# Optimization experiments

Measured on AMD Instinct MI355X. Metric: run time of the kernel, lower is better.

The kernel has to match this reference:

```python
import jax, jax.numpy as jnp
import numpy as np

B, V, C, H, W, D = 1, 3, 32, 320, 320, 32


def setup_inputs() -> dict:
    key = jax.random.key(0)
    ks = jax.random.split(key, 14)
    feats = jax.random.normal(ks[0], (B, V, C, H, W), jnp.float32)
    # Valid pinhole projections: P = [[K @ [R|t]], [0,0,0,1]], identity rotation,
    # horizontal baselines sized so the warp stays mostly in-image over the depth range.
    K = np.array([[400.0, 0.0, W / 2.0], [0.0, 400.0, H / 2.0], [0.0, 0.0, 1.0]])
    mats = []
    for tx in (0.0, 100.0, -100.0):
        Rt = np.eye(4)
        Rt[0, 3] = tx
        P = np.eye(4)
        P[:3, :4] = K @ Rt[:3, :4]
        mats.append(P)
    proj = jnp.asarray(np.broadcast_to(np.stack(mats)[None], (B, V, 4, 4)).copy(), jnp.float32)
    planes = jnp.linspace(425.0, 935.0, D, dtype=jnp.float32)
    depth_values = jnp.broadcast_to(planes[None, :, None, None], (B, D, H, W)).astype(jnp.float32)
    s = 0.05  # small init so exp(reg_cost) stays well-scaled
    W0 = s * jax.random.normal(ks[1], (8, C, 3, 3), jnp.float32)
    Ws1 = s * jax.random.normal(ks[2], (8, 8, 3, 3), jnp.float32)
    W1 = s * jax.random.normal(ks[3], (16, 8, 3, 3), jnp.float32)
    Ws2 = s * jax.random.normal(ks[4], (16, 16, 3, 3), jnp.float32)
    W2 = s * jax.random.normal(ks[5], (32, 16, 3, 3), jnp.float32)
    Ws3 = s * jax.random.normal(ks[6], (32, 32, 3, 3), jnp.float32)
    W3 = s * jax.random.normal(ks[7], (64, 32, 3, 3), jnp.float32)
    Ws4 = s * jax.random.normal(ks[8], (64, 64, 3, 3), jnp.float32)
    U4 = s * jax.random.normal(ks[9], (32, 64, 1, 1), jnp.float32)
    U3 = s * jax.random.normal(ks[10], (16, 32, 1, 1), jnp.float32)
    U2 = s * jax.random.normal(ks[11], (8, 16, 1, 1), jnp.float32)
    Wout = s * jax.random.normal(ks[12], (1, 8, 3, 3), jnp.float32)
    return dict(feats=feats, proj=proj, depth_values=depth_values, W0=W0, Ws1=Ws1,
                W1=W1, Ws2=Ws2, W2=W2, Ws3=Ws3, W3=W3, Ws4=Ws4, U4=U4, U3=U3, U2=U2, Wout=Wout)


def _conv(x, w, stride=1):
    return jax.lax.conv_general_dilated(x, w, (stride, stride), 'SAME',
                                        dimension_numbers=('NCHW', 'OIHW', 'NCHW'))


def _up2(x):
    return jnp.repeat(jnp.repeat(x, 2, axis=2), 2, axis=3)


def _bilinear(img, x, y):
    # img [C,H,W]; x,y [N] pixel coords; zero padding, align_corners semantics
    Cc, Hh, Ww = img.shape
    x0 = jnp.floor(x)
    y0 = jnp.floor(y)
    wx = x - x0
    wy = y - y0

    def tap(xi, yi):
        valid = ((xi >= 0) & (xi <= Ww - 1) & (yi >= 0) & (yi <= Hh - 1)).astype(img.dtype)
        xc = jnp.clip(xi, 0, Ww - 1).astype(jnp.int32)
        yc = jnp.clip(yi, 0, Hh - 1).astype(jnp.int32)
        return img[:, yc, xc] * valid  # [C,N]

    return (tap(x0, y0) * (1 - wx) * (1 - wy) + tap(x0 + 1, y0) * wx * (1 - wy)
            + tap(x0, y0 + 1) * (1 - wx) * wy + tap(x0 + 1, y0 + 1) * wx * wy)


def _forward(feats, proj, depth_values, W0, Ws1, W1, Ws2, W2, Ws3, W3, Ws4, U4, U3, U2, Wout):
    Bn, Vn, Cn, Hn, Wn = feats.shape
    Dn = depth_values.shape[1]
    N = Hn * Wn
    relu = jax.nn.relu
    ref = feats[:, 0]
    ref_sq = ref * ref
    # Precompute per-src-view rotated pixel rays and translations.
    inv_ref = jnp.linalg.inv(proj[:, 0])                       # [B,4,4]
    rel = jnp.einsum('bvij,bjk->bvik', proj[:, 1:], inv_ref)   # [B,V-1,4,4]
    rot, trans = rel[:, :, :3, :3], rel[:, :, :3, 3]
    ys, xs = jnp.meshgrid(jnp.arange(Hn), jnp.arange(Wn), indexing='ij')
    pix = jnp.stack([xs.ravel(), ys.ravel(), jnp.ones(N)], 0).astype(feats.dtype)  # [3,N]
    rot_pix = jnp.einsum('bvij,jn->bvin', rot, pix)            # [B,V-1,3,N]

    def regularize(x, s1, s2, s3, s4):
        c1 = relu(_conv(x, W0) + _conv(s1, Ws1))
        c2 = relu(_conv(c1, W1, 2) + _conv(s2, Ws2))
        c3 = relu(_conv(c2, W2, 2) + _conv(s3, Ws3))
        c4 = relu(_conv(c3, W3, 2) + _conv(s4, Ws4))
        u3 = c3 + _up2(_conv(c4, U4))
        u2 = c2 + _up2(_conv(u3, U3))
        u1 = c1 + _up2(_conv(u2, U2))
        return _conv(u1, Wout), c1, c2, c3, c4

    def step(carry, depth_slice):  # depth_slice [B,H,W]
        s1, s2, s3, s4, exp_sum, depth_img, max_prob = carry
        vol_sum, vol_sq = ref, ref_sq
        dflat = depth_slice.reshape(Bn, 1, N)
        for v in range(Vn - 1):
            xyz = rot_pix[:, v] * dflat + trans[:, v, :, None]   # [B,3,N]
            px = xyz[:, 0] / xyz[:, 2]
            py = xyz[:, 1] / xyz[:, 2]
            warped = jax.vmap(_bilinear)(feats[:, v + 1], px, py).reshape(Bn, Cn, Hn, Wn)
            vol_sum = vol_sum + warped
            vol_sq = vol_sq + warped * warped
        variance = vol_sq / Vn - (vol_sum / Vn) ** 2
        cost, s1, s2, s3, s4 = regularize(variance, s1, s2, s3, s4)
        prob = jnp.exp(cost)                                     # [B,1,H,W]
        max_prob = jnp.maximum(max_prob, prob)                   # == flag*prob + (1-flag)*max
        depth_img = depth_img + depth_slice[:, None] * prob
        exp_sum = exp_sum + prob
        return (s1, s2, s3, s4, exp_sum, depth_img, max_prob), None

    z = lambda c, h, w: jnp.zeros((Bn, c, h, w), feats.dtype)
    init = (z(8, Hn, Wn), z(16, Hn // 2, Wn // 2), z(32, Hn // 4, Wn // 4), z(64, Hn // 8, Wn // 8),
            z(1, Hn, Wn), z(1, Hn, Wn), z(1, Hn, Wn))
    carry, _ = jax.lax.scan(step, init, jnp.moveaxis(depth_values, 1, 0))
    _, _, _, _, exp_sum, depth_img, max_prob = carry
    es = exp_sum + 1e-10
    depth_map = (depth_img / es)[:, 0]
    prob_map = (max_prob / es)[:, 0]
    return jnp.stack([depth_map, prob_map], axis=1)  # [B,2,H,W]


def reference(feats, proj, depth_values, W0, Ws1, W1, Ws2, W2, Ws3, W3, Ws4, U4, U3, U2, Wout):
    return _forward(feats, proj, depth_values, W0, Ws1, W1, Ws2, W2, Ws3, W3, Ws4, U4, U3, U2, Wout)
```

## Files before the change

### kernel.cpp

```cpp
#include <hip/hip_runtime.h>
#include <hip/hip_fp16.h>
#include <math.h>

#define HH 320
#define WW 320
#define NP (HH*WW)
#define CC 32
#define DD 32

#define H2 160
#define W2 160
#define N2 (H2*W2)
#define H4 80
#define W4 80
#define N4 (H4*W4)
#define H8 40
#define W8 40
#define N8 (H8*W8)

#define HALO 18
#define NHALO (HALO*HALO)

#define C1SZ (8*NP)
#define C2SZ (16*N2)
#define C3SZ (32*N4)
#define C4SZ (64*N8)

#define SMEM_FLOATS 5344

#define OFF_REL   0
#define OFF_C1R   64
#define OFF_C2R   (OFF_C1R + 5*C1SZ)
#define OFF_C3R   (OFF_C2R + 4*C2SZ)
#define OFF_C4R   (OFF_C3R + 3*C3SZ)
#define OFF_ESUM  (OFF_C4R + 2*C4SZ)
#define OFF_DIMG  (OFF_ESUM + NP)
#define OFF_MAXP  (OFF_DIMG + NP)
#define OFF_ACCE  (OFF_MAXP + NP)
#define OFF_FT    OFF_ACCE
#define OFF_END   (OFF_FT + (3*CC*NP)/2)

__global__ void k_prep(const float* __restrict__ proj, float* __restrict__ rel) {
    if (threadIdx.x != 0 || blockIdx.x != 0) return;
    float a[4][4], inv[4][4];
#pragma unroll
    for (int i = 0; i < 4; i++)
#pragma unroll
        for (int j = 0; j < 4; j++) {
            a[i][j] = proj[i*4 + j];
            inv[i][j] = (i == j) ? 1.0f : 0.0f;
        }
#pragma unroll
    for (int c = 0; c < 4; c++) {
        float s = 1.0f / a[c][c];
#pragma unroll
        for (int j = 0; j < 4; j++) { a[c][j] *= s; inv[c][j] *= s; }
#pragma unroll
        for (int r = 0; r < 4; r++) if (r != c) {
            float f = a[r][c];
#pragma unroll
            for (int j = 0; j < 4; j++) {
                a[r][j] -= f * a[c][j];
                inv[r][j] -= f * inv[c][j];
            }
        }
    }
#pragma unroll
    for (int v = 1; v < 3; v++) {
        const float* P = proj + v*16;
        float rm[3][4];
#pragma unroll
        for (int i = 0; i < 3; i++)
#pragma unroll
            for (int j = 0; j < 4; j++) {
                float s = 0.0f;
#pragma unroll
                for (int k = 0; k < 4; k++) s += P[i*4 + k] * inv[k][j];
                rm[i][j] = s;
            }
        float* o = rel + (v-1)*12;
        o[0]=rm[0][0]; o[1]=rm[0][1]; o[2]=rm[0][2];
        o[3]=rm[1][0]; o[4]=rm[1][1]; o[5]=rm[1][2];
        o[6]=rm[2][0]; o[7]=rm[2][1]; o[8]=rm[2][2];
        o[9]=rm[0][3]; o[10]=rm[1][3]; o[11]=rm[2][3];
    }
}

__global__ __launch_bounds__(256) void k_transpose(const float* __restrict__ feats,
                                                   __half* __restrict__ featsT) {
    __shared__ float lds[32][65];
    int g = blockIdx.x;
    int v = g / 1600;
    int p0 = (g - v*1600) * 64;
    const float* src = feats + (size_t)v*CC*NP + p0;
    for (int i = threadIdx.x; i < 32*64; i += 256) {
        int c = i >> 6, pp = i & 63;
        lds[c][pp] = src[(size_t)c*NP + pp];
    }
    __syncthreads();
    __half* dst = featsT + ((size_t)v*NP + p0)*32;
    int pp = threadIdx.x >> 2, cq = (threadIdx.x & 3) * 8;
    __half2 h[4];
#pragma unroll
    for (int j = 0; j < 4; j++)
        h[j] = __floats2half2_rn(lds[cq+2*j][pp], lds[cq+2*j+1][pp]);
    *(float4*)(dst + (size_t)pp*32 + cq) = *(float4*)h;
}

__device__ __forceinline__ void set_line_h(const __half* base, float* s) {
    const float4* q = (const float4*)base;
#pragma unroll
    for (int i = 0; i < 4; i++) {
        float4 raw = q[i];
        const __half2* h2 = (const __half2*)&raw;
#pragma unroll
        for (int j = 0; j < 4; j++) {
            float2 f = __half22float2(h2[j]);
            s[i*8 + 2*j]     = f.x;
            s[i*8 + 2*j + 1] = f.y;
        }
    }
}
__device__ __forceinline__ void acc_line_h(const __half* base, float w, float* t) {
    const float4* q = (const float4*)base;
#pragma unroll
    for (int i = 0; i < 4; i++) {
        float4 raw = q[i];
        const __half2* h2 = (const __half2*)&raw;
#pragma unroll
        for (int j = 0; j < 4; j++) {
            float2 f = __half22float2(h2[j]);
            t[i*8 + 2*j]     += f.x * w;
            t[i*8 + 2*j + 1] += f.y * w;
        }
    }
}

__device__ __forceinline__ int band_tile(int blk) {
    return (blk & 7) * 50 + (blk >> 3);
}


__device__ void stageA(int blk, int d, int useT,
        const float* __restrict__ feats, const __half* __restrict__ featsT,
        const float* __restrict__ rel,
        const float* __restrict__ depthv, const float* __restrict__ c1r,
        const float* __restrict__ W0, const float* __restrict__ Ws1,
        float* smem) {
    __half2* pbuf = (__half2*)smem;
    float* fbuf = smem;
    const float* dslice = depthv + (size_t)d * NP;
    const float* s1 = c1r + (size_t)((d+4)%5) * C1SZ;
    float* c1out = (float*)c1r + (size_t)(d%5) * C1SZ;

    int L = band_tile(blk);
    int bx = L % 20, by = L / 20;
    int ox0 = bx*16, oy0 = by*16;

    const float* f1 = feats + CC*NP;
    const float* f2 = feats + 2*CC*NP;
    const __half* fT0 = featsT;
    const __half* fT1 = featsT + (size_t)CC*NP;
    const __half* fT2 = featsT + (size_t)2*CC*NP;
    const float inv3 = 1.0f / 3.0f;

    int opx = threadIdx.x & 15, opy = threadIdx.x >> 4;
    int obase = opy*HALO + opx;
    int outp = (oy0 + opy)*WW + ox0 + opx;

    for (int s = 0; s < 2; s++) {
        int hp = threadIdx.x + s*256;
        if (hp >= NHALO) break;
        int hy = hp / HALO, hx = hp - hy*HALO;
        int gy = oy0 + hy - 1, gx = ox0 + hx - 1;
        if (gy < 0 || gy >= HH || gx < 0 || gx >= WW) {
            __half2 z = __floats2half2_rn(0.0f, 0.0f);
#pragma unroll 8
            for (int c = 0; c < 16; c++) pbuf[c*NHALO + hp] = z;
            continue;
        }
        int p = gy*WW + gx;
        float depth = dslice[p];
        float fx = (float)gx, fy = (float)gy;
        int offs[8]; float wts[8];
#pragma unroll
        for (int v = 0; v < 2; v++) {
            const float* r = rel + v*12;
            float X = (r[0]*fx + r[1]*fy + r[2]) * depth + r[9];
            float Y = (r[3]*fx + r[4]*fy + r[5]) * depth + r[10];
            float Z = (r[6]*fx + r[7]*fy + r[8]) * depth + r[11];
            float iz = 1.0f / Z;
            float px = X * iz, py = Y * iz;
            float x0f = floorf(px), y0f = floorf(py);
            float wx = px - x0f, wy = py - y0f;
            int x0 = (int)x0f, y0 = (int)y0f;
#pragma unroll
            for (int t = 0; t < 4; t++) {
                int xi = x0 + (t & 1), yi = y0 + (t >> 1);
                float wgt = ((t & 1) ? wx : 1.0f - wx) * ((t >> 1) ? wy : 1.0f - wy);
                bool valid = (xi >= 0) && (xi <= WW-1) && (yi >= 0) && (yi <= HH-1);
                int xc = min(max(xi, 0), WW-1);
                int yc = min(max(yi, 0), HH-1);
                offs[v*4 + t] = yc*WW + xc;
                wts[v*4 + t] = valid ? wgt : 0.0f;
            }
        }

        float var[32];
        if (useT) {
            float sum[32], sq[32], t[32];
            set_line_h(fT0 + ((size_t)p << 5), sum);
#pragma unroll
            for (int c = 0; c < 32; c++) sq[c] = sum[c]*sum[c];
#pragma unroll
            for (int c = 0; c < 32; c++) t[c] = 0.0f;
#pragma unroll
            for (int tp = 0; tp < 4; tp++)
                acc_line_h(fT1 + ((size_t)offs[tp] << 5), wts[tp], t);
#pragma unroll
            for (int c = 0; c < 32; c++) { sum[c] += t[c]; sq[c] += t[c]*t[c]; }
#pragma unroll
            for (int c = 0; c < 32; c++) t[c] = 0.0f;
#pragma unroll
            for (int tp = 0; tp < 4; tp++)
                acc_line_h(fT2 + ((size_t)offs[4+tp] << 5), wts[4+tp], t);
#pragma unroll
            for (int c = 0; c < 32; c++) { sum[c] += t[c]; sq[c] += t[c]*t[c]; }
#pragma unroll
            for (int c = 0; c < 32; c++) {
                float m = sum[c] * inv3;
                var[c] = sq[c] * inv3 - m*m;
            }
        } else {
            for (int c = 0; c < 32; c++) {
                float rv = feats[c*NP + p];
                const float* b1 = f1 + c*NP;
                float t1 = b1[offs[0]]*wts[0] + b1[offs[1]]*wts[1]
                         + b1[offs[2]]*wts[2] + b1[offs[3]]*wts[3];
                const float* b2 = f2 + c*NP;
                float t2 = b2[offs[4]]*wts[4] + b2[offs[5]]*wts[5]
                         + b2[offs[6]]*wts[6] + b2[offs[7]]*wts[7];
                float sum = rv + t1 + t2;
                float sq  = rv*rv + t1*t1 + t2*t2;
                float m = sum * inv3;
                var[c] = sq * inv3 - m*m;
            }
        }
#pragma unroll
        for (int c = 0; c < 16; c++)
            pbuf[c*NHALO + hp] = __floats2half2_rn(var[2*c], var[2*c+1]);
    }
    __syncthreads();

    float acc[8];
#pragma unroll
    for (int o = 0; o < 8; o++) acc[o] = 0.0f;

    for (int cp = 0; cp < 16; cp++) {
        float t0[9], t1[9];
#pragma unroll
        for (int ky = 0; ky < 3; ky++)
#pragma unroll
            for (int kx = 0; kx < 3; kx++) {
                __half2 h = pbuf[cp*NHALO + obase + ky*HALO + kx];
                t0[ky*3+kx] = __low2float(h);
                t1[ky*3+kx] = __high2float(h);
            }
#pragma unroll
        for (int o = 0; o < 8; o++) {
            const float* w0 = W0 + (o*32 + 2*cp)*9;
            float a = acc[o];
#pragma unroll
            for (int k = 0; k < 9; k++) a += t0[k] * w0[k];
#pragma unroll
            for (int k = 0; k < 9; k++) a += t1[k] * w0[9 + k];
            acc[o] = a;
        }
    }
    __syncthreads();

    for (int hp = threadIdx.x; hp < NHALO; hp += 256) {
        int hy = hp / HALO, hx = hp - hy*HALO;
        int gy = oy0 + hy - 1, gx = ox0 + hx - 1;
        bool v = (gy >= 0) && (gy < HH) && (gx >= 0) && (gx < WW);
        int p = v ? gy*WW + gx : 0;
#pragma unroll
        for (int c = 0; c < 8; c++) fbuf[c*NHALO + hp] = v ? s1[c*NP + p] : 0.0f;
    }
    __syncthreads();
    for (int ci = 0; ci < 8; ci++) {
        float t[9];
#pragma unroll
        for (int ky = 0; ky < 3; ky++)
#pragma unroll
            for (int kx = 0; kx < 3; kx++) t[ky*3+kx] = fbuf[ci*NHALO + obase + ky*HALO + kx];
#pragma unroll
        for (int o = 0; o < 8; o++) {
            const float* w = Ws1 + (o*8 + ci)*9;
            float a = acc[o];
#pragma unroll
            for (int k = 0; k < 9; k++) a += t[k] * w[k];
            acc[o] = a;
        }
    }
#pragma unroll
    for (int o = 0; o < 8; o++) c1out[o*NP + outp] = fmaxf(acc[o], 0.0f);
}

__device__ void stageB(int blk, int d,
        const float* __restrict__ c1r, const float* __restrict__ c2r_,
        const float* __restrict__ W1, const float* __restrict__ Ws2) {
    const float* c1 = c1r + (size_t)(d%5) * C1SZ;
    const float* s2 = c2r_ + (size_t)((d+3)%4) * C2SZ;
    float* c2 = (float*)c2r_ + (size_t)(d%4) * C2SZ;
    int p = (blk % 100)*256 + threadIdx.x;
    if (p >= N2) return;
    int og = blk / 100;
    int y = p / W2, x = p - y*W2;
    int offsA[9]; float mskA[9];
#pragma unroll
    for (int k = 0; k < 9; k++) {
        int yy = 2*y + k/3, xx = 2*x + k%3;
        bool v = (yy < HH) && (xx < WW);
        offsA[k] = v ? yy*WW + xx : 0;
        mskA[k] = v ? 1.0f : 0.0f;
    }
    int offsB[9]; float mskB[9];
#pragma unroll
    for (int k = 0; k < 9; k++) {
        int yy = y + k/3 - 1, xx = x + k%3 - 1;
        bool v = (yy >= 0) && (yy < H2) && (xx >= 0) && (xx < W2);
        offsB[k] = v ? yy*W2 + xx : 0;
        mskB[k] = v ? 1.0f : 0.0f;
    }
    float acc[8];
#pragma unroll
    for (int o = 0; o < 8; o++) acc[o] = 0.0f;
    for (int ci = 0; ci < 8; ci++) {
        const float* b = c1 + ci*NP;
        float t[9];
#pragma unroll
        for (int k = 0; k < 9; k++) t[k] = b[offsA[k]] * mskA[k];
#pragma unroll
        for (int o = 0; o < 8; o++) {
            const float* w = W1 + ((og*8 + o)*8 + ci)*9;
            float a = acc[o];
#pragma unroll
            for (int k = 0; k < 9; k++) a += t[k] * w[k];
            acc[o] = a;
        }
    }
    for (int ci = 0; ci < 16; ci++) {
        const float* b = s2 + ci*N2;
        float t[9];
#pragma unroll
        for (int k = 0; k < 9; k++) t[k] = b[offsB[k]] * mskB[k];
#pragma unroll
        for (int o = 0; o < 8; o++) {
            const float* w = Ws2 + ((og*8 + o)*16 + ci)*9;
            float a = acc[o];
#pragma unroll
            for (int k = 0; k < 9; k++) a += t[k] * w[k];
            acc[o] = a;
        }
    }
#pragma unroll
    for (int o = 0; o < 8; o++) c2[(og*8 + o)*N2 + p] = fmaxf(acc[o], 0.0f);
}

__device__ void stageC(int blk, int d,
        const float* __restrict__ c2r_, const float* __restrict__ c3r_,
        const float* __restrict__ W2w, const float* __restrict__ Ws3) {
    const float* c2 = c2r_ + (size_t)(d%4) * C2SZ;
    const float* s3 = c3r_ + (size_t)((d+2)%3) * C3SZ;
    float* c3 = (float*)c3r_ + (size_t)(d%3) * C3SZ;
    int p = (blk % 25)*256 + threadIdx.x;
    if (p >= N4) return;
    int og = blk / 25;
    int y = p / W4, x = p - y*W4;
    int offsA[9]; float mskA[9];
#pragma unroll
    for (int k = 0; k < 9; k++) {
        int yy = 2*y + k/3, xx = 2*x + k%3;
        bool v = (yy < H2) && (xx < W2);
        offsA[k] = v ? yy*W2 + xx : 0;
        mskA[k] = v ? 1.0f : 0.0f;
    }
    int offsB[9]; float mskB[9];
#pragma unroll
    for (int k = 0; k < 9; k++) {
        int yy = y + k/3 - 1, xx = x + k%3 - 1;
        bool v = (yy >= 0) && (yy < H4) && (xx >= 0) && (xx < W4);
        offsB[k] = v ? yy*W4 + xx : 0;
        mskB[k] = v ? 1.0f : 0.0f;
    }
    float acc[8];
#pragma unroll
    for (int o = 0; o < 8; o++) acc[o] = 0.0f;
    for (int ci = 0; ci < 16; ci++) {
        const float* b = c2 + ci*N2;
        float t[9];
#pragma unroll
        for (int k = 0; k < 9; k++) t[k] = b[offsA[k]] * mskA[k];
#pragma unroll
        for (int o = 0; o < 8; o++) {
            const float* w = W2w + ((og*8 + o)*16 + ci)*9;
            float a = acc[o];
#pragma unroll
            for (int k = 0; k < 9; k++) a += t[k] * w[k];
            acc[o] = a;
        }
    }
    for (int ci = 0; ci < 32; ci++) {
        const float* b = s3 + ci*N4;
        float t[9];
#pragma unroll
        for (int k = 0; k < 9; k++) t[k] = b[offsB[k]] * mskB[k];
#pragma unroll
        for (int o = 0; o < 8; o++) {
            const float* w = Ws3 + ((og*8 + o)*32 + ci)*9;
            float a = acc[o];
#pragma unroll
            for (int k = 0; k < 9; k++) a += t[k] * w[k];
            acc[o] = a;
        }
    }
#pragma unroll
    for (int o = 0; o < 8; o++) c3[(og*8 + o)*N4 + p] = fmaxf(acc[o], 0.0f);
}

__device__ void stageD(int blk, int d,
        const float* __restrict__ c3r_, const float* __restrict__ c4r_,
        const float* __restrict__ W3w, const float* __restrict__ Ws4) {
    const float* c3 = c3r_ + (size_t)(d%3) * C3SZ;
    const float* s4 = c4r_ + (size_t)((d+1)%2) * C4SZ;
    float* c4 = (float*)c4r_ + (size_t)(d%2) * C4SZ;
    int p = (blk % 7)*256 + threadIdx.x;
    if (p >= N8) return;
    int og = blk / 7;
    int y = p / W8, x = p - y*W8;
    int offsA[9]; float mskA[9];
#pragma unroll
    for (int k = 0; k < 9; k++) {
        int yy = 2*y + k/3, xx = 2*x + k%3;
        bool v = (yy < H4) && (xx < W4);
        offsA[k] = v ? yy*W4 + xx : 0;
        mskA[k] = v ? 1.0f : 0.0f;
    }
    int offsB[9]; float mskB[9];
#pragma unroll
    for (int k = 0; k < 9; k++) {
        int yy = y + k/3 - 1, xx = x + k%3 - 1;
        bool v = (yy >= 0) && (yy < H8) && (xx >= 0) && (xx < W8);
        offsB[k] = v ? yy*W8 + xx : 0;
        mskB[k] = v ? 1.0f : 0.0f;
    }
    float acc[8];
#pragma unroll
    for (int o = 0; o < 8; o++) acc[o] = 0.0f;
    for (int ci = 0; ci < 32; ci++) {
        const float* b = c3 + ci*N4;
        float t[9];
#pragma unroll
        for (int k = 0; k < 9; k++) t[k] = b[offsA[k]] * mskA[k];
#pragma unroll
        for (int o = 0; o < 8; o++) {
            const float* w = W3w + ((og*8 + o)*32 + ci)*9;
            float a = acc[o];
#pragma unroll
            for (int k = 0; k < 9; k++) a += t[k] * w[k];
            acc[o] = a;
        }
    }
    for (int ci = 0; ci < 64; ci++) {
        const float* b = s4 + ci*N8;
        float t[9];
#pragma unroll
        for (int k = 0; k < 9; k++) t[k] = b[offsB[k]] * mskB[k];
#pragma unroll
        for (int o = 0; o < 8; o++) {
            const float* w = Ws4 + ((og*8 + o)*64 + ci)*9;
            float a = acc[o];
#pragma unroll
            for (int k = 0; k < 9; k++) a += t[k] * w[k];
            acc[o] = a;
        }
    }
#pragma unroll
    for (int o = 0; o < 8; o++) c4[(og*8 + o)*N8 + p] = fmaxf(acc[o], 0.0f);
}

__device__ void stageU(int blk, int d,
        const float* __restrict__ c1r, const float* __restrict__ c2r_,
        const float* __restrict__ c3r_, const float* __restrict__ c4r_,
        const float* __restrict__ U4, const float* __restrict__ U3,
        const float* __restrict__ U2, const float* __restrict__ Wout,
        const float* __restrict__ depthv,
        float* __restrict__ exp_sum, float* __restrict__ depth_img,
        float* __restrict__ max_prob, float* smem) {
    const float* c1 = c1r + (size_t)(d%5) * C1SZ;
    const float* c2 = c2r_ + (size_t)(d%4) * C2SZ;
    const float* c3 = c3r_ + (size_t)(d%3) * C3SZ;
    const float* c4 = c4r_ + (size_t)(d%2) * C4SZ;
    const float* dslice = depthv + (size_t)d * NP;
    float* u3s = smem;
    float* u2s = smem + 32*36;
    float* u1s = smem + 32*36 + 16*100;

    int L = band_tile(blk);
    int bx = L % 20, by = L / 20;
    int ox0 = bx*16, oy0 = by*16;
    int qy0 = (oy0 >> 2) - 1, qx0 = (ox0 >> 2) - 1;
    int hy0 = (oy0 >> 1) - 1, hx0 = (ox0 >> 1) - 1;

    for (int i = threadIdx.x; i < 32*36; i += 256) {
        int ch = i / 36, pp = i - ch*36;
        int y4 = qy0 + pp/6, x4 = qx0 + pp%6;
        int y4c = min(max(y4, 0), H4-1), x4c = min(max(x4, 0), W4-1);
        int pl = (y4c >> 1)*W8 + (x4c >> 1);
        const float* w = U4 + ch*64;
        float s = c3[ch*N4 + y4c*W4 + x4c];
#pragma unroll 8
        for (int ci = 0; ci < 64; ci++) s += c4[ci*N8 + pl] * w[ci];
        u3s[ch*36 + pp] = s;
    }
    __syncthreads();
    for (int i = threadIdx.x; i < 16*100; i += 256) {
        int ch = i / 100, pp = i - ch*100;
        int y2 = hy0 + pp/10, x2 = hx0 + pp%10;
        int y2c = min(max(y2, 0), H2-1), x2c = min(max(x2, 0), W2-1);
        int ly = (y2c >> 1) - qy0, lx = (x2c >> 1) - qx0;
        const float* w = U3 + ch*32;
        float s = c2[ch*N2 + y2c*W2 + x2c];
#pragma unroll 8
        for (int ci = 0; ci < 32; ci++) s += u3s[ci*36 + ly*6 + lx] * w[ci];
        u2s[ch*100 + pp] = s;
    }
    __syncthreads();
    for (int i = threadIdx.x; i < 8*NHALO; i += 256) {
        int ch = i / NHALO, pp = i - ch*NHALO;
        int gy = oy0 + pp/HALO - 1, gx = ox0 + pp%HALO - 1;
        float s = 0.0f;
        if (gy >= 0 && gy < HH && gx >= 0 && gx < WW) {
            int ly = (gy >> 1) - hy0, lx = (gx >> 1) - hx0;
            const float* w = U2 + ch*16;
            s = c1[ch*NP + gy*WW + gx];
#pragma unroll
            for (int ci = 0; ci < 16; ci++) s += u2s[ci*100 + ly*10 + lx] * w[ci];
        }
        u1s[ch*NHALO + pp] = s;
    }
    __syncthreads();
    int px = threadIdx.x & 15, py = threadIdx.x >> 4;
    int base = py*HALO + px;
    float cost = 0.0f;
#pragma unroll
    for (int ci = 0; ci < 8; ci++) {
        const float* w = Wout + ci*9;
#pragma unroll
        for (int ky = 0; ky < 3; ky++)
#pragma unroll
            for (int kx = 0; kx < 3; kx++)
                cost += u1s[ci*NHALO + base + ky*HALO + kx] * w[ky*3 + kx];
    }
    int p = (oy0 + py)*WW + ox0 + px;
    float prob = expf(cost);
    exp_sum[p] += prob;
    depth_img[p] += dslice[p] * prob;
    max_prob[p] = fmaxf(max_prob[p], prob);
}

__global__ __launch_bounds__(256) void k_uber(
        int t, int useT,
        const float* __restrict__ feats, const __half* __restrict__ featsT,
        const float* __restrict__ rel,
        const float* __restrict__ depthv,
        const float* __restrict__ W0, const float* __restrict__ Ws1,
        const float* __restrict__ W1, const float* __restrict__ Ws2,
        const float* __restrict__ W2w, const float* __restrict__ Ws3,
        const float* __restrict__ W3w, const float* __restrict__ Ws4,
        const float* __restrict__ U4, const float* __restrict__ U3,
        const float* __restrict__ U2, const float* __restrict__ Wout,
        float* __restrict__ c1r, float* __restrict__ c2r,
        float* __restrict__ c3r, float* __restrict__ c4r,
        float* __restrict__ esum, float* __restrict__ dimg,
        float* __restrict__ maxp) {
    __shared__ float smem[SMEM_FLOATS];
    int b = blockIdx.x;
    if (b < 400) {
        int d = t;
        if (d < DD) stageA(b, d, useT, feats, featsT, rel, depthv, c1r, W0, Ws1, smem);
    } else if (b < 600) {
        int d = t - 1;
        if (d >= 0 && d < DD) stageB(b - 400, d, c1r, c2r, W1, Ws2);
    } else if (b < 700) {
        int d = t - 2;
        if (d >= 0 && d < DD) stageC(b - 600, d, c2r, c3r, W2w, Ws3);
    } else if (b < 756) {
        int d = t - 3;
        if (d >= 0 && d < DD) stageD(b - 700, d, c3r, c4r, W3w, Ws4);
    } else {
        int d = t - 4;
        if (d >= 0 && d < DD)
            stageU(b - 756, d, c1r, c2r, c3r, c4r, U4, U3, U2, Wout, depthv,
                   esum, dimg, maxp, smem);
    }
}

__global__ __launch_bounds__(256) void k_final(
        const float* __restrict__ exp_sum, const float* __restrict__ depth_img,
        const float* __restrict__ max_prob, float* __restrict__ out) {
    int p = blockIdx.x*256 + threadIdx.x;
    if (p >= NP) return;
    float es = exp_sum[p] + 1e-10f;
    out[p] = depth_img[p] / es;
    out[NP + p] = max_prob[p] / es;
}

extern "C" void kernel_launch(void* const* d_in, const int* in_sizes, int n_in,
                              void* d_out, int out_size, void* d_ws, size_t ws_size,
                              hipStream_t stream) {
    const float* feats = (const float*)d_in[0];
    const float* proj  = (const float*)d_in[1];
    const float* depthv= (const float*)d_in[2];
    const float* W0  = (const float*)d_in[3];
    const float* Ws1 = (const float*)d_in[4];
    const float* W1  = (const float*)d_in[5];
    const float* Ws2 = (const float*)d_in[6];
    const float* W2w = (const float*)d_in[7];
    const float* Ws3 = (const float*)d_in[8];
    const float* W3w = (const float*)d_in[9];
    const float* Ws4 = (const float*)d_in[10];
    const float* U4  = (const float*)d_in[11];
    const float* U3  = (const float*)d_in[12];
    const float* U2  = (const float*)d_in[13];
    const float* Wout= (const float*)d_in[14];

    float* ws = (float*)d_ws;
    float* rel  = ws + OFF_REL;
    float* c1r  = ws + OFF_C1R;
    float* c2r  = ws + OFF_C2R;
    float* c3r  = ws + OFF_C3R;
    float* c4r  = ws + OFF_C4R;
    float* esum = ws + OFF_ESUM;
    float* dimg = ws + OFF_DIMG;
    float* maxp = ws + OFF_MAXP;

    int useT = (ws_size >= (size_t)OFF_END * sizeof(float)) ? 1 : 0;
    __half* featsT = (__half*)(useT ? (ws + OFF_FT) : ws);

    hipMemsetAsync(c1r, 0, (size_t)(OFF_ACCE - OFF_C1R) * sizeof(float), stream);
    k_prep<<<1, 1, 0, stream>>>(proj, rel);
    if (useT)
        k_transpose<<<dim3(3*1600), 256, 0, stream>>>(feats, featsT);

    for (int t = 0; t < DD + 4; t++) {
        k_uber<<<dim3(1156), 256, 0, stream>>>(t, useT, feats, featsT, rel, depthv,
            W0, Ws1, W1, Ws2, W2w, Ws3, W3w, Ws4, U4, U3, U2, Wout,
            c1r, c2r, c3r, c4r, esum, dimg, maxp);
    }
    k_final<<<dim3(400), 256, 0, stream>>>(esum, dimg, maxp, (float*)d_out);
}
```

Baseline: 3.176 ms.

## Split variance warp out of conv stage into separate pipelined stage

Stage A's homography warp and variance computation now run as their own pipeline stage. Each thread handles one pixel and 16 channels, writing an fp16 variance volume into a double-buffered workspace. The conv stage then just loads halo tiles from that buffer, which removes the redundant warp work the old code did on halo pixels and raises parallelism in the first stage. In exchange the pipeline gains one more step and one more launch, the grid grows, and each depth slice needs an extra global write and read of roughly 6.5 MB.

```diff
diff --git a/kernel.cpp b/kernel.cpp
--- a/kernel.cpp
+++ b/kernel.cpp
@@ -37,7 +37,9 @@
 #define OFF_DIMG  (OFF_ESUM + NP)
 #define OFF_MAXP  (OFF_DIMG + NP)
 #define OFF_ACCE  (OFF_MAXP + NP)
-#define OFF_FT    OFF_ACCE
+#define VARSZ_F   ((CC*NP)/2)
+#define OFF_VARR  OFF_ACCE
+#define OFF_FT    (OFF_VARR + 2*VARSZ_F)
 #define OFF_END   (OFF_FT + (3*CC*NP)/2)
 
 __global__ void k_prep(const float* __restrict__ proj, float* __restrict__ rel) {
@@ -107,10 +109,10 @@
     *(float4*)(dst + (size_t)pp*32 + cq) = *(float4*)h;
 }
 
-__device__ __forceinline__ void set_line_h(const __half* base, float* s) {
+__device__ __forceinline__ void set_hline16(const __half* base, float* s) {
     const float4* q = (const float4*)base;
 #pragma unroll
-    for (int i = 0; i < 4; i++) {
+    for (int i = 0; i < 2; i++) {
         float4 raw = q[i];
         const __half2* h2 = (const __half2*)&raw;
 #pragma unroll
@@ -121,10 +123,10 @@
         }
     }
 }
-__device__ __forceinline__ void acc_line_h(const __half* base, float w, float* t) {
+__device__ __forceinline__ void acc_hline16(const __half* base, float w, float* t) {
     const float4* q = (const float4*)base;
 #pragma unroll
-    for (int i = 0; i < 4; i++) {
+    for (int i = 0; i < 2; i++) {
         float4 raw = q[i];
         const __half2* h2 = (const __half2*)&raw;
 #pragma unroll
@@ -136,119 +138,127 @@
     }
 }
 
-__device__ __forceinline__ int band_tile(int blk) {
-    return (blk & 7) * 50 + (blk >> 3);
-}
-
-
-__device__ void stageA(int blk, int d, int useT,
+__device__ __forceinline__ int band_tile(int blk)  { return (blk & 7) * 50  + (blk >> 3); }
+__device__ __forceinline__ int band_chunk(int blk) { return (blk & 7) * 100 + (blk >> 3); }
+
+
+__device__ void stageAvar(int blk, int d, int useT,
         const float* __restrict__ feats, const __half* __restrict__ featsT,
-        const float* __restrict__ rel,
-        const float* __restrict__ depthv, const float* __restrict__ c1r,
+        const float* __restrict__ rel, const float* __restrict__ depthv,
+        __half* __restrict__ varR) {
+    int chunk = band_chunk(blk);
+    int p = chunk * 128 + (threadIdx.x & 127);
+    int half = threadIdx.x >> 7;
+    int cb = half * 16;
+    const float* dslice = depthv + (size_t)d * NP;
+    float depth = dslice[p];
+    int gy = p / WW, gx = p - gy*WW;
+    float fx = (float)gx, fy = (float)gy;
+    int offs[8]; float wts[8];
+#pragma unroll
+    for (int v = 0; v < 2; v++) {
+        const float* r = rel + v*12;
+        float X = (r[0]*fx + r[1]*fy + r[2]) * depth + r[9];
+        float Y = (r[3]*fx + r[4]*fy + r[5]) * depth + r[10];
+        float Z = (r[6]*fx + r[7]*fy + r[8]) * depth + r[11];
+        float iz = 1.0f / Z;
+        float px = X * iz, py = Y * iz;
+        float x0f = floorf(px), y0f = floorf(py);
+        float wx = px - x0f, wy = py - y0f;
+        int x0 = (int)x0f, y0 = (int)y0f;
+#pragma unroll
+        for (int t = 0; t < 4; t++) {
+            int xi = x0 + (t & 1), yi = y0 + (t >> 1);
+            float wgt = ((t & 1) ? wx : 1.0f - wx) * ((t >> 1) ? wy : 1.0f - wy);
+            bool valid = (xi >= 0) && (xi <= WW-1) && (yi >= 0) && (yi <= HH-1);
+            int xc = min(max(xi, 0), WW-1);
+            int yc = min(max(yi, 0), HH-1);
+            offs[v*4 + t] = yc*WW + xc;
+            wts[v*4 + t] = valid ? wgt : 0.0f;
+        }
+    }
+
+    const float inv3 = 1.0f / 3.0f;
+    float sum[16], sq[16], t[16], var[16];
+    if (useT) {
+        const __half* fT0 = featsT;
+        const __half* fT1 = featsT + (size_t)CC*NP;
+        const __half* fT2 = featsT + (size_t)2*CC*NP;
+        set_hline16(fT0 + ((size_t)p << 5) + cb, sum);
+#pragma unroll
+        for (int c = 0; c < 16; c++) sq[c] = sum[c]*sum[c];
+#pragma unroll
+        for (int c = 0; c < 16; c++) t[c] = 0.0f;
+#pragma unroll
+        for (int tp = 0; tp < 4; tp++)
+            acc_hline16(fT1 + ((size_t)offs[tp] << 5) + cb, wts[tp], t);
+#pragma unroll
+        for (int c = 0; c < 16; c++) { sum[c] += t[c]; sq[c] += t[c]*t[c]; }
+#pragma unroll
+        for (int c = 0; c < 16; c++) t[c] = 0.0f;
+#pragma unroll
+        for (int tp = 0; tp < 4; tp++)
+            acc_hline16(fT2 + ((size_t)offs[4+tp] << 5) + cb, wts[4+tp], t);
+#pragma unroll
+        for (int c = 0; c < 16; c++) { sum[c] += t[c]; sq[c] += t[c]*t[c]; }
+    } else {
+        const float* f1 = feats + CC*NP;
+        const float* f2 = feats + 2*CC*NP;
+        for (int c = 0; c < 16; c++) {
+            float rv = feats[(cb+c)*NP + p];
+            const float* b1 = f1 + (cb+c)*NP;
+            float t1 = b1[offs[0]]*wts[0] + b1[offs[1]]*wts[1]
+                     + b1[offs[2]]*wts[2] + b1[offs[3]]*wts[3];
+            const float* b2 = f2 + (cb+c)*NP;
+            float t2 = b2[offs[4]]*wts[4] + b2[offs[5]]*wts[5]
+                     + b2[offs[6]]*wts[6] + b2[offs[7]]*wts[7];
+            sum[c] = rv + t1 + t2;
+            sq[c]  = rv*rv + t1*t1 + t2*t2;
+        }
+    }
+#pragma unroll
+    for (int c = 0; c < 16; c++) {
+        float m = sum[c] * inv3;
+        var[c] = sq[c] * inv3 - m*m;
+    }
+    __half2 o[8];
+#pragma unroll
+    for (int c = 0; c < 8; c++) o[c] = __floats2half2_rn(var[2*c], var[2*c+1]);
+    float4* dst = (float4*)(varR + (size_t)(d & 1) * (size_t)CC * NP
+                                  + ((size_t)p << 5) + cb);
+    dst[0] = ((float4*)o)[0];
+    dst[1] = ((float4*)o)[1];
+}
+
+__device__ void stageAconv(int blk, int d,
+        const __half* __restrict__ varR, const float* __restrict__ c1r,
         const float* __restrict__ W0, const float* __restrict__ Ws1,
         float* smem) {
     __half2* pbuf = (__half2*)smem;
     float* fbuf = smem;
-    const float* dslice = depthv + (size_t)d * NP;
     const float* s1 = c1r + (size_t)((d+4)%5) * C1SZ;
     float* c1out = (float*)c1r + (size_t)(d%5) * C1SZ;
+    const __half* vsrc = varR + (size_t)(d & 1) * (size_t)CC * NP;
 
     int L = band_tile(blk);
     int bx = L % 20, by = L / 20;
     int ox0 = bx*16, oy0 = by*16;
 
-    const float* f1 = feats + CC*NP;
-    const float* f2 = feats + 2*CC*NP;
-    const __half* fT0 = featsT;
-    const __half* fT1 = featsT + (size_t)CC*NP;
-    const __half* fT2 = featsT + (size_t)2*CC*NP;
-    const float inv3 = 1.0f / 3.0f;
-
     int opx = threadIdx.x & 15, opy = threadIdx.x >> 4;
     int obase = opy*HALO + opx;
     int outp = (oy0 + opy)*WW + ox0 + opx;
 
-    for (int s = 0; s < 2; s++) {
-        int hp = threadIdx.x + s*256;
-        if (hp >= NHALO) break;
+    for (int i = threadIdx.x; i < NHALO*4; i += 256) {
+        int hp = i >> 2, q = i & 3;
         int hy = hp / HALO, hx = hp - hy*HALO;
         int gy = oy0 + hy - 1, gx = ox0 + hx - 1;
-        if (gy < 0 || gy >= HH || gx < 0 || gx >= WW) {
-            __half2 z = __floats2half2_rn(0.0f, 0.0f);
-#pragma unroll 8
-            for (int c = 0; c < 16; c++) pbuf[c*NHALO + hp] = z;
-            continue;
-        }
-        int p = gy*WW + gx;
-        float depth = dslice[p];
-        float fx = (float)gx, fy = (float)gy;
-        int offs[8]; float wts[8];
-#pragma unroll
-        for (int v = 0; v < 2; v++) {
-            const float* r = rel + v*12;
-            float X = (r[0]*fx + r[1]*fy + r[2]) * depth + r[9];
-            float Y = (r[3]*fx + r[4]*fy + r[5]) * depth + r[10];
-            float Z = (r[6]*fx + r[7]*fy + r[8]) * depth + r[11];
-            float iz = 1.0f / Z;
-            float px = X * iz, py = Y * iz;
-            float x0f = floorf(px), y0f = floorf(py);
-            float wx = px - x0f, wy = py - y0f;
-            int x0 = (int)x0f, y0 = (int)y0f;
-#pragma unroll
-            for (int t = 0; t < 4; t++) {
-                int xi = x0 + (t & 1), yi = y0 + (t >> 1);
-                float wgt = ((t & 1) ? wx : 1.0f - wx) * ((t >> 1) ? wy : 1.0f - wy);
-                bool valid = (xi >= 0) && (xi <= WW-1) && (yi >= 0) && (yi <= HH-1);
-                int xc = min(max(xi, 0), WW-1);
-                int yc = min(max(yi, 0), HH-1);
-                offs[v*4 + t] = yc*WW + xc;
-                wts[v*4 + t] = valid ? wgt : 0.0f;
-            }
-        }
-
-        float var[32];
-        if (useT) {
-            float sum[32], sq[32], t[32];
-            set_line_h(fT0 + ((size_t)p << 5), sum);
-#pragma unroll
-            for (int c = 0; c < 32; c++) sq[c] = sum[c]*sum[c];
-#pragma unroll
-            for (int c = 0; c < 32; c++) t[c] = 0.0f;
-#pragma unroll
-            for (int tp = 0; tp < 4; tp++)
-                acc_line_h(fT1 + ((size_t)offs[tp] << 5), wts[tp], t);
-#pragma unroll
-            for (int c = 0; c < 32; c++) { sum[c] += t[c]; sq[c] += t[c]*t[c]; }
-#pragma unroll
-            for (int c = 0; c < 32; c++) t[c] = 0.0f;
-#pragma unroll
-            for (int tp = 0; tp < 4; tp++)
-                acc_line_h(fT2 + ((size_t)offs[4+tp] << 5), wts[4+tp], t);
-#pragma unroll
-            for (int c = 0; c < 32; c++) { sum[c] += t[c]; sq[c] += t[c]*t[c]; }
-#pragma unroll
-            for (int c = 0; c < 32; c++) {
-                float m = sum[c] * inv3;
-                var[c] = sq[c] * inv3 - m*m;
-            }
-        } else {
-            for (int c = 0; c < 32; c++) {
-                float rv = feats[c*NP + p];
-                const float* b1 = f1 + c*NP;
-                float t1 = b1[offs[0]]*wts[0] + b1[offs[1]]*wts[1]
-                         + b1[offs[2]]*wts[2] + b1[offs[3]]*wts[3];
-                const float* b2 = f2 + c*NP;
-                float t2 = b2[offs[4]]*wts[4] + b2[offs[5]]*wts[5]
-                         + b2[offs[6]]*wts[6] + b2[offs[7]]*wts[7];
-                float sum = rv + t1 + t2;
-                float sq  = rv*rv + t1*t1 + t2*t2;
-                float m = sum * inv3;
-                var[c] = sq * inv3 - m*m;
-            }
-        }
-#pragma unroll
-        for (int c = 0; c < 16; c++)
-            pbuf[c*NHALO + hp] = __floats2half2_rn(var[2*c], var[2*c+1]);
+        float4 v4 = make_float4(0.0f, 0.0f, 0.0f, 0.0f);
+        if (gy >= 0 && gy < HH && gx >= 0 && gx < WW)
+            v4 = *(const float4*)(vsrc + ((size_t)(gy*WW + gx) << 5) + q*8);
+        const __half2* h2 = (const __half2*)&v4;
+#pragma unroll
+        for (int j = 0; j < 4; j++)
+            pbuf[(q*4 + j)*NHALO + hp] = h2[j];
     }
     __syncthreads();
 
@@ -584,25 +594,28 @@
         float* __restrict__ c1r, float* __restrict__ c2r,
         float* __restrict__ c3r, float* __restrict__ c4r,
         float* __restrict__ esum, float* __restrict__ dimg,
-        float* __restrict__ maxp) {
+        float* __restrict__ maxp, __half* __restrict__ varR) {
     __shared__ float smem[SMEM_FLOATS];
     int b = blockIdx.x;
-    if (b < 400) {
+    if (b < 800) {
         int d = t;
-        if (d < DD) stageA(b, d, useT, feats, featsT, rel, depthv, c1r, W0, Ws1, smem);
-    } else if (b < 600) {
+        if (d < DD) stageAvar(b, d, useT, feats, featsT, rel, depthv, varR);
+    } else if (b < 1200) {
         int d = t - 1;
-        if (d >= 0 && d < DD) stageB(b - 400, d, c1r, c2r, W1, Ws2);
-    } else if (b < 700) {
+        if (d >= 0 && d < DD) stageAconv(b - 800, d, varR, c1r, W0, Ws1, smem);
+    } else if (b < 1400) {
         int d = t - 2;
-        if (d >= 0 && d < DD) stageC(b - 600, d, c2r, c3r, W2w, Ws3);
-    } else if (b < 756) {
+        if (d >= 0 && d < DD) stageB(b - 1200, d, c1r, c2r, W1, Ws2);
+    } else if (b < 1500) {
         int d = t - 3;
-        if (d >= 0 && d < DD) stageD(b - 700, d, c3r, c4r, W3w, Ws4);
+        if (d >= 0 && d < DD) stageC(b - 1400, d, c2r, c3r, W2w, Ws3);
+    } else if (b < 1556) {
+        int d = t - 4;
+        if (d >= 0 && d < DD) stageD(b - 1500, d, c3r, c4r, W3w, Ws4);
     } else {
-        int d = t - 4;
+        int d = t - 5;
         if (d >= 0 && d < DD)
-            stageU(b - 756, d, c1r, c2r, c3r, c4r, U4, U3, U2, Wout, depthv,
+            stageU(b - 1556, d, c1r, c2r, c3r, c4r, U4, U3, U2, Wout, depthv,
                    esum, dimg, maxp, smem);
     }
 }
@@ -645,6 +658,7 @@
     float* esum = ws + OFF_ESUM;
     float* dimg = ws + OFF_DIMG;
     float* maxp = ws + OFF_MAXP;
+    __half* varR = (__half*)(ws + OFF_VARR);
 
     int useT = (ws_size >= (size_t)OFF_END * sizeof(float)) ? 1 : 0;
     __half* featsT = (__half*)(useT ? (ws + OFF_FT) : ws);
@@ -654,10 +668,10 @@
     if (useT)
         k_transpose<<<dim3(3*1600), 256, 0, stream>>>(feats, featsT);
 
-    for (int t = 0; t < DD + 4; t++) {
-        k_uber<<<dim3(1156), 256, 0, stream>>>(t, useT, feats, featsT, rel, depthv,
+    for (int t = 0; t < DD + 5; t++) {
+        k_uber<<<dim3(1956), 256, 0, stream>>>(t, useT, feats, featsT, rel, depthv,
             W0, Ws1, W1, Ws2, W2w, Ws3, W3w, Ws4, U4, U3, U2, Wout,
-            c1r, c2r, c3r, c4r, esum, dimg, maxp);
+            c1r, c2r, c3r, c4r, esum, dimg, maxp, varR);
     }
     k_final<<<dim3(400), 256, 0, stream>>>(esum, dimg, maxp, (float*)d_out);
 }
```

Result: slower. 6.088 ms (+91.7%).

## Split stage A into 16x8 tiles with output-channel split across thread halves

Applied to the files above, without the earlier changes.

Stage A tiles shrink from 16x16 to 16x8, so twice as many blocks (800) run the warp/variance and first conv stage. The 180-pixel halo is now covered in a single pass by 256 threads, and the two halves of the block each compute 4 of the 8 output channels. This is meant to shorten the critical-path stage A block and spread its work across more CUs per pipeline step. The cost is more halo recomputation, since 180 halo pixels serve 128 outputs instead of 324 serving 256, and the launch grows to 1556 blocks.

```diff
diff --git a/kernel.cpp b/kernel.cpp
--- a/kernel.cpp
+++ b/kernel.cpp
@@ -17,6 +17,12 @@
 #define H8 40
 #define W8 40
 #define N8 (H8*W8)
+
+#define TAW 16
+#define TAH 8
+#define HAW 18
+#define HAH 10
+#define NHA (HAW*HAH)
 
 #define HALO 18
 #define NHALO (HALO*HALO)
@@ -136,9 +142,8 @@
     }
 }
 
-__device__ __forceinline__ int band_tile(int blk) {
-    return (blk & 7) * 50 + (blk >> 3);
-}
+__device__ __forceinline__ int band_tileU(int blk) { return (blk & 7) * 50  + (blk >> 3); }
+__device__ __forceinline__ int band_tileA(int blk) { return (blk & 7) * 100 + (blk >> 3); }
 
 
 __device__ void stageA(int blk, int d, int useT,
@@ -153,9 +158,9 @@
     const float* s1 = c1r + (size_t)((d+4)%5) * C1SZ;
     float* c1out = (float*)c1r + (size_t)(d%5) * C1SZ;
 
-    int L = band_tile(blk);
+    int L = band_tileA(blk);
     int bx = L % 20, by = L / 20;
-    int ox0 = bx*16, oy0 = by*16;
+    int ox0 = bx*TAW, oy0 = by*TAH;
 
     const float* f1 = feats + CC*NP;
     const float* f2 = feats + 2*CC*NP;
@@ -164,97 +169,96 @@
     const __half* fT2 = featsT + (size_t)2*CC*NP;
     const float inv3 = 1.0f / 3.0f;
 
-    int opx = threadIdx.x & 15, opy = threadIdx.x >> 4;
-    int obase = opy*HALO + opx;
-    int outp = (oy0 + opy)*WW + ox0 + opx;
-
-    for (int s = 0; s < 2; s++) {
-        int hp = threadIdx.x + s*256;
-        if (hp >= NHALO) break;
-        int hy = hp / HALO, hx = hp - hy*HALO;
+    int hp = threadIdx.x;
+    if (hp < NHA) {
+        int hy = hp / HAW, hx = hp - hy*HAW;
         int gy = oy0 + hy - 1, gx = ox0 + hx - 1;
         if (gy < 0 || gy >= HH || gx < 0 || gx >= WW) {
             __half2 z = __floats2half2_rn(0.0f, 0.0f);
 #pragma unroll 8
-            for (int c = 0; c < 16; c++) pbuf[c*NHALO + hp] = z;
-            continue;
-        }
-        int p = gy*WW + gx;
-        float depth = dslice[p];
-        float fx = (float)gx, fy = (float)gy;
-        int offs[8]; float wts[8];
-#pragma unroll
-        for (int v = 0; v < 2; v++) {
-            const float* r = rel + v*12;
-            float X = (r[0]*fx + r[1]*fy + r[2]) * depth + r[9];
-            float Y = (r[3]*fx + r[4]*fy + r[5]) * depth + r[10];
-            float Z = (r[6]*fx + r[7]*fy + r[8]) * depth + r[11];
-            float iz = 1.0f / Z;
-            float px = X * iz, py = Y * iz;
-            float x0f = floorf(px), y0f = floorf(py);
-            float wx = px - x0f, wy = py - y0f;
-            int x0 = (int)x0f, y0 = (int)y0f;
-#pragma unroll
-            for (int t = 0; t < 4; t++) {
-                int xi = x0 + (t & 1), yi = y0 + (t >> 1);
-                float wgt = ((t & 1) ? wx : 1.0f - wx) * ((t >> 1) ? wy : 1.0f - wy);
-                bool valid = (xi >= 0) && (xi <= WW-1) && (yi >= 0) && (yi <= HH-1);
-                int xc = min(max(xi, 0), WW-1);
-                int yc = min(max(yi, 0), HH-1);
-                offs[v*4 + t] = yc*WW + xc;
-                wts[v*4 + t] = valid ? wgt : 0.0f;
+            for (int c = 0; c < 16; c++) pbuf[c*NHA + hp] = z;
+        } else {
+            int p = gy*WW + gx;
+            float depth = dslice[p];
+            float fx = (float)gx, fy = (float)gy;
+            int offs[8]; float wts[8];
+#pragma unroll
+            for (int v = 0; v < 2; v++) {
+                const float* r = rel + v*12;
+                float X = (r[0]*fx + r[1]*fy + r[2]) * depth + r[9];
+                float Y = (r[3]*fx + r[4]*fy + r[5]) * depth + r[10];
+                float Z = (r[6]*fx + r[7]*fy + r[8]) * depth + r[11];
+                float iz = 1.0f / Z;
+                float px = X * iz, py = Y * iz;
+                float x0f = floorf(px), y0f = floorf(py);
+                float wx = px - x0f, wy = py - y0f;
+                int x0 = (int)x0f, y0 = (int)y0f;
+#pragma unroll
+                for (int t = 0; t < 4; t++) {
+                    int xi = x0 + (t & 1), yi = y0 + (t >> 1);
+                    float wgt = ((t & 1) ? wx : 1.0f - wx) * ((t >> 1) ? wy : 1.0f - wy);
+                    bool valid = (xi >= 0) && (xi <= WW-1) && (yi >= 0) && (yi <= HH-1);
+                    int xc = min(max(xi, 0), WW-1);
+                    int yc = min(max(yi, 0), HH-1);
+                    offs[v*4 + t] = yc*WW + xc;
+                    wts[v*4 + t] = valid ? wgt : 0.0f;
+                }
             }
-        }
-
-        float var[32];
-        if (useT) {
-            float sum[32], sq[32], t[32];
-            set_line_h(fT0 + ((size_t)p << 5), sum);
-#pragma unroll
-            for (int c = 0; c < 32; c++) sq[c] = sum[c]*sum[c];
-#pragma unroll
-            for (int c = 0; c < 32; c++) t[c] = 0.0f;
-#pragma unroll
-            for (int tp = 0; tp < 4; tp++)
-                acc_line_h(fT1 + ((size_t)offs[tp] << 5), wts[tp], t);
-#pragma unroll
-            for (int c = 0; c < 32; c++) { sum[c] += t[c]; sq[c] += t[c]*t[c]; }
-#pragma unroll
-            for (int c = 0; c < 32; c++) t[c] = 0.0f;
-#pragma unroll
-            for (int tp = 0; tp < 4; tp++)
-                acc_line_h(fT2 + ((size_t)offs[4+tp] << 5), wts[4+tp], t);
-#pragma unroll
-            for (int c = 0; c < 32; c++) { sum[c] += t[c]; sq[c] += t[c]*t[c]; }
-#pragma unroll
-            for (int c = 0; c < 32; c++) {
-                float m = sum[c] * inv3;
-                var[c] = sq[c] * inv3 - m*m;
+
+            float var[32];
+            if (useT) {
+                float sum[32], sq[32], t[32];
+                set_line_h(fT0 + ((size_t)p << 5), sum);
+#pragma unroll
+                for (int c = 0; c < 32; c++) sq[c] = sum[c]*sum[c];
+#pragma unroll
+                for (int c = 0; c < 32; c++) t[c] = 0.0f;
+#pragma unroll
+                for (int tp = 0; tp < 4; tp++)
+                    acc_line_h(fT1 + ((size_t)offs[tp] << 5), wts[tp], t);
+#pragma unroll
+                for (int c = 0; c < 32; c++) { sum[c] += t[c]; sq[c] += t[c]*t[c]; }
+#pragma unroll
+                for (int c = 0; c < 32; c++) t[c] = 0.0f;
+#pragma unroll
+                for (int tp = 0; tp < 4; tp++)
+                    acc_line_h(fT2 + ((size_t)offs[4+tp] << 5), wts[4+tp], t);
+#pragma unroll
+                for (int c = 0; c < 32; c++) { sum[c] += t[c]; sq[c] += t[c]*t[c]; }
+#pragma unroll
+                for (int c = 0; c < 32; c++) {
+                    float m = sum[c] * inv3;
+                    var[c] = sq[c] * inv3 - m*m;
+                }
+            } else {
+                for (int c = 0; c < 32; c++) {
+                    float rv = feats[c*NP + p];
+                    const float* b1 = f1 + c*NP;
+                    float t1 = b1[offs[0]]*wts[0] + b1[offs[1]]*wts[1]
+                             + b1[offs[2]]*wts[2] + b1[offs[3]]*wts[3];
+                    const float* b2 = f2 + c*NP;
+                    float t2 = b2[offs[4]]*wts[4] + b2[offs[5]]*wts[5]
+                             + b2[offs[6]]*wts[6] + b2[offs[7]]*wts[7];
+                    float sum = rv + t1 + t2;
+                    float sq  = rv*rv + t1*t1 + t2*t2;
+                    float m = sum * inv3;
+                    var[c] = sq * inv3 - m*m;
+                }
             }
-        } else {
-            for (int c = 0; c < 32; c++) {
-                float rv = feats[c*NP + p];
-                const float* b1 = f1 + c*NP;
-                float t1 = b1[offs[0]]*wts[0] + b1[offs[1]]*wts[1]
-                         + b1[offs[2]]*wts[2] + b1[offs[3]]*wts[3];
-                const float* b2 = f2 + c*NP;
-                float t2 = b2[offs[4]]*wts[4] + b2[offs[5]]*wts[5]
-                         + b2[offs[6]]*wts[6] + b2[offs[7]]*wts[7];
-                float sum = rv + t1 + t2;
-                float sq  = rv*rv + t1*t1 + t2*t2;
-                float m = sum * inv3;
-                var[c] = sq * inv3 - m*m;
-            }
-        }
-#pragma unroll
-        for (int c = 0; c < 16; c++)
-            pbuf[c*NHALO + hp] = __floats2half2_rn(var[2*c], var[2*c+1]);
+#pragma unroll
+            for (int c = 0; c < 16; c++)
+                pbuf[c*NHA + hp] = __floats2half2_rn(var[2*c], var[2*c+1]);
+        }
     }
     __syncthreads();
 
-    float acc[8];
-#pragma unroll
-    for (int o = 0; o < 8; o++) acc[o] = 0.0f;
+    int px_ = threadIdx.x & 127;
+    int og  = threadIdx.x >> 7;
+    int opy = px_ >> 4, opx = px_ & 15;
+    int obase = opy*HAW + opx;
+    float acc[4];
+#pragma unroll
+    for (int o = 0; o < 4; o++) acc[o] = 0.0f;
 
     for (int cp = 0; cp < 16; cp++) {
         float t0[9], t1[9];
@@ -262,13 +266,13 @@
         for (int ky = 0; ky < 3; ky++)
 #pragma unroll
             for (int kx = 0; kx < 3; kx++) {
-                __half2 h = pbuf[cp*NHALO + obase + ky*HALO + kx];
+                __half2 h = pbuf[cp*NHA + obase + ky*HAW + kx];
                 t0[ky*3+kx] = __low2float(h);
                 t1[ky*3+kx] = __high2float(h);
             }
 #pragma unroll
-        for (int o = 0; o < 8; o++) {
-            const float* w0 = W0 + (o*32 + 2*cp)*9;
+        for (int o = 0; o < 4; o++) {
+            const float* w0 = W0 + ((og*4 + o)*32 + 2*cp)*9;
             float a = acc[o];
 #pragma unroll
             for (int k = 0; k < 9; k++) a += t0[k] * w0[k];
@@ -279,13 +283,13 @@
     }
     __syncthreads();
 
-    for (int hp = threadIdx.x; hp < NHALO; hp += 256) {
-        int hy = hp / HALO, hx = hp - hy*HALO;
+    if (hp < NHA) {
+        int hy = hp / HAW, hx = hp - hy*HAW;
         int gy = oy0 + hy - 1, gx = ox0 + hx - 1;
         bool v = (gy >= 0) && (gy < HH) && (gx >= 0) && (gx < WW);
         int p = v ? gy*WW + gx : 0;
 #pragma unroll
-        for (int c = 0; c < 8; c++) fbuf[c*NHALO + hp] = v ? s1[c*NP + p] : 0.0f;
+        for (int c = 0; c < 8; c++) fbuf[c*NHA + hp] = v ? s1[c*NP + p] : 0.0f;
     }
     __syncthreads();
     for (int ci = 0; ci < 8; ci++) {
@@ -293,18 +297,19 @@
 #pragma unroll
         for (int ky = 0; ky < 3; ky++)
 #pragma unroll
-            for (int kx = 0; kx < 3; kx++) t[ky*3+kx] = fbuf[ci*NHALO + obase + ky*HALO + kx];
-#pragma unroll
-        for (int o = 0; o < 8; o++) {
-            const float* w = Ws1 + (o*8 + ci)*9;
+            for (int kx = 0; kx < 3; kx++) t[ky*3+kx] = fbuf[ci*NHA + obase + ky*HAW + kx];
+#pragma unroll
+        for (int o = 0; o < 4; o++) {
+            const float* w = Ws1 + ((og*4 + o)*8 + ci)*9;
             float a = acc[o];
 #pragma unroll
             for (int k = 0; k < 9; k++) a += t[k] * w[k];
             acc[o] = a;
         }
     }
-#pragma unroll
-    for (int o = 0; o < 8; o++) c1out[o*NP + outp] = fmaxf(acc[o], 0.0f);
+    int outp = (oy0 + opy)*WW + ox0 + opx;
+#pragma unroll
+    for (int o = 0; o < 4; o++) c1out[(og*4 + o)*NP + outp] = fmaxf(acc[o], 0.0f);
 }
 
 __device__ void stageB(int blk, int d,
@@ -507,7 +512,7 @@
     float* u2s = smem + 32*36;
     float* u1s = smem + 32*36 + 16*100;
 
-    int L = band_tile(blk);
+    int L = band_tileU(blk);
     int bx = L % 20, by = L / 20;
     int ox0 = bx*16, oy0 = by*16;
     int qy0 = (oy0 >> 2) - 1, qx0 = (ox0 >> 2) - 1;
@@ -587,22 +592,22 @@
         float* __restrict__ maxp) {
     __shared__ float smem[SMEM_FLOATS];
     int b = blockIdx.x;
-    if (b < 400) {
+    if (b < 800) {
         int d = t;
         if (d < DD) stageA(b, d, useT, feats, featsT, rel, depthv, c1r, W0, Ws1, smem);
-    } else if (b < 600) {
+    } else if (b < 1000) {
         int d = t - 1;
-        if (d >= 0 && d < DD) stageB(b - 400, d, c1r, c2r, W1, Ws2);
-    } else if (b < 700) {
+        if (d >= 0 && d < DD) stageB(b - 800, d, c1r, c2r, W1, Ws2);
+    } else if (b < 1100) {
         int d = t - 2;
-        if (d >= 0 && d < DD) stageC(b - 600, d, c2r, c3r, W2w, Ws3);
-    } else if (b < 756) {
+        if (d >= 0 && d < DD) stageC(b - 1000, d, c2r, c3r, W2w, Ws3);
+    } else if (b < 1156) {
         int d = t - 3;
-        if (d >= 0 && d < DD) stageD(b - 700, d, c3r, c4r, W3w, Ws4);
+        if (d >= 0 && d < DD) stageD(b - 1100, d, c3r, c4r, W3w, Ws4);
     } else {
         int d = t - 4;
         if (d >= 0 && d < DD)
-            stageU(b - 756, d, c1r, c2r, c3r, c4r, U4, U3, U2, Wout, depthv,
+            stageU(b - 1156, d, c1r, c2r, c3r, c4r, U4, U3, U2, Wout, depthv,
                    esum, dimg, maxp, smem);
     }
 }
@@ -655,7 +660,7 @@
         k_transpose<<<dim3(3*1600), 256, 0, stream>>>(feats, featsT);
 
     for (int t = 0; t < DD + 4; t++) {
-        k_uber<<<dim3(1156), 256, 0, stream>>>(t, useT, feats, featsT, rel, depthv,
+        k_uber<<<dim3(1556), 256, 0, stream>>>(t, useT, feats, featsT, rel, depthv,
             W0, Ws1, W1, Ws2, W2w, Ws3, W3w, Ws4, U4, U3, U2, Wout,
             c1r, c2r, c3r, c4r, esum, dimg, maxp);
     }
```

Result: slower. 3.330 ms (+4.9%).

## Remap uber-kernel blocks to CU/XCD-aware slots for balanced stage placement

Applied to the files above, without the earlier changes.

Replaces the linear block-to-stage mapping with one based on blockIdx modulo 256 and slot index. Each pipeline stage gets a contiguous range of CU indices, and spatial bands stay within one XCD. The goal is to spread each stage's work evenly across compute units and keep neighbouring tiles sharing an XCD's L2. The grid grows to 1280 blocks, and some of them exit immediately.

```diff
diff --git a/kernel.cpp b/kernel.cpp
--- a/kernel.cpp
+++ b/kernel.cpp
@@ -136,12 +136,8 @@
     }
 }
 
-__device__ __forceinline__ int band_tile(int blk) {
-    return (blk & 7) * 50 + (blk >> 3);
-}
-
-
-__device__ void stageA(int blk, int d, int useT,
+
+__device__ void stageA(int L, int d, int useT,
         const float* __restrict__ feats, const __half* __restrict__ featsT,
         const float* __restrict__ rel,
         const float* __restrict__ depthv, const float* __restrict__ c1r,
@@ -153,7 +149,6 @@
     const float* s1 = c1r + (size_t)((d+4)%5) * C1SZ;
     float* c1out = (float*)c1r + (size_t)(d%5) * C1SZ;
 
-    int L = band_tile(blk);
     int bx = L % 20, by = L / 20;
     int ox0 = bx*16, oy0 = by*16;
 
@@ -490,7 +485,7 @@
     for (int o = 0; o < 8; o++) c4[(og*8 + o)*N8 + p] = fmaxf(acc[o], 0.0f);
 }
 
-__device__ void stageU(int blk, int d,
+__device__ void stageU(int L, int d,
         const float* __restrict__ c1r, const float* __restrict__ c2r_,
         const float* __restrict__ c3r_, const float* __restrict__ c4r_,
         const float* __restrict__ U4, const float* __restrict__ U3,
@@ -507,7 +502,6 @@
     float* u2s = smem + 32*36;
     float* u1s = smem + 32*36 + 16*100;
 
-    int L = band_tile(blk);
     int bx = L % 20, by = L / 20;
     int ox0 = bx*16, oy0 = by*16;
     int qy0 = (oy0 >> 2) - 1, qx0 = (ox0 >> 2) - 1;
@@ -586,24 +580,35 @@
         float* __restrict__ esum, float* __restrict__ dimg,
         float* __restrict__ maxp) {
     __shared__ float smem[SMEM_FLOATS];
-    int b = blockIdx.x;
-    if (b < 400) {
+    int cu   = blockIdx.x & 255;
+    int slot = blockIdx.x >> 8;
+    int xcd  = cu & 7;
+    if (cu < 104) {
         int d = t;
-        if (d < DD) stageA(b, d, useT, feats, featsT, rel, depthv, c1r, W0, Ws1, smem);
-    } else if (b < 600) {
+        if (d >= DD || slot >= 4) return;
+        int bl = (cu >> 3)*4 + slot;
+        if (bl >= 50) return;
+        stageA(xcd*50 + bl, d, useT, feats, featsT, rel, depthv, c1r, W0, Ws1, smem);
+    } else if (cu < 144) {
         int d = t - 1;
-        if (d >= 0 && d < DD) stageB(b - 400, d, c1r, c2r, W1, Ws2);
-    } else if (b < 700) {
+        if (d < 0 || d >= DD) return;
+        stageB((cu - 104)*5 + slot, d, c1r, c2r, W1, Ws2);
+    } else if (cu < 164) {
         int d = t - 2;
-        if (d >= 0 && d < DD) stageC(b - 600, d, c2r, c3r, W2w, Ws3);
-    } else if (b < 756) {
+        if (d < 0 || d >= DD) return;
+        stageC((cu - 144)*5 + slot, d, c2r, c3r, W2w, Ws3);
+    } else if (cu < 176) {
         int d = t - 3;
-        if (d >= 0 && d < DD) stageD(b - 700, d, c3r, c4r, W3w, Ws4);
+        if (d < 0 || d >= DD) return;
+        int bl = (cu - 164)*5 + slot;
+        if (bl >= 56) return;
+        stageD(bl, d, c3r, c4r, W3w, Ws4);
     } else {
         int d = t - 4;
-        if (d >= 0 && d < DD)
-            stageU(b - 756, d, c1r, c2r, c3r, c4r, U4, U3, U2, Wout, depthv,
-                   esum, dimg, maxp, smem);
+        if (d < 0 || d >= DD) return;
+        int bl = ((cu - 176) >> 3)*5 + slot;
+        stageU(xcd*50 + bl, d, c1r, c2r, c3r, c4r, U4, U3, U2, Wout, depthv,
+               esum, dimg, maxp, smem);
     }
 }
 
@@ -655,7 +660,7 @@
         k_transpose<<<dim3(3*1600), 256, 0, stream>>>(feats, featsT);
 
     for (int t = 0; t < DD + 4; t++) {
-        k_uber<<<dim3(1156), 256, 0, stream>>>(t, useT, feats, featsT, rel, depthv,
+        k_uber<<<dim3(5*256), 256, 0, stream>>>(t, useT, feats, featsT, rel, depthv,
             W0, Ws1, W1, Ws2, W2w, Ws3, W3w, Ws4, U4, U3, U2, Wout,
             c1r, c2r, c3r, c4r, esum, dimg, maxp);
     }
```

New measurement: 7.164 ms. 2.26x slower.
